# Kernel optimization log

Hardware: AMD Instinct MI355X
Metric: run time of the kernel (lower is better)

Reference implementation:

```python
import jax, jax.numpy as jnp
import numpy as np


def _dsepconv(inp, vert, horiz, offx, offy, mask):
    # inp: [B,C,H,W]; vert/horiz: [B,F,H,W]; offx/offy/mask: [B,F*F,H,W]
    B, C, H, W = inp.shape
    F = vert.shape[1]
    FF = F * F
    dt = inp.dtype
    k = jnp.arange(FF)
    ki = (k // F).astype(dt)   # vertical tap index i
    kj = (k % F).astype(dt)    # horizontal tap index j
    half = jnp.asarray((F - 1) / 2.0, dt)
    ys = jnp.arange(H, dtype=dt)
    xs = jnp.arange(W, dtype=dt)
    # per-pixel deformable sample positions, [B,FF,H,W]
    py = offy + ys[None, None, :, None] + (ki - half)[None, :, None, None]
    px = offx + xs[None, None, None, :] + (kj - half)[None, :, None, None]
    py = jnp.clip(py, 0.0, H - 1)
    px = jnp.clip(px, 0.0, W - 1)
    y0f = jnp.floor(py)
    x0f = jnp.floor(px)
    wy = py - y0f   # bilinear fractional weights
    wx = px - x0f
    y0 = y0f.astype(jnp.int32)
    x0 = x0f.astype(jnp.int32)
    y1 = jnp.minimum(y0 + 1, H - 1)
    x1 = jnp.minimum(x0 + 1, W - 1)

    inp_flat = inp.reshape(B, C, H * W)

    def gather(yi, xi):
        # flat spatial gather per batch element -> [B,C,FF,H,W]
        idx = (yi * W + xi).reshape(B, FF * H * W)
        g = jax.vmap(lambda im, ix: im[:, ix])(inp_flat, idx)
        return g.reshape(B, C, FF, H, W)

    g00 = gather(y0, x0)
    g01 = gather(y0, x1)
    g10 = gather(y1, x0)
    g11 = gather(y1, x1)
    wy_ = wy[:, None]  # [B,1,FF,H,W]
    wx_ = wx[:, None]
    samp = (g00 * (1 - wy_) * (1 - wx_)
            + g01 * (1 - wy_) * wx_
            + g10 * wy_ * (1 - wx_)
            + g11 * wy_ * wx_)  # [B,C,FF,H,W]
    # separable mask-weighted tap weights: vert[i]*horiz[j]*mask[k]
    wtap = vert[:, k // F] * horiz[:, k % F] * mask  # [B,FF,H,W]
    return jnp.einsum('bkhw,bckhw->bchw', wtap, samp)


def setup_inputs() -> dict:
    key = jax.random.key(0)
    ks = jax.random.split(key, 6)
    B, C, H, W, F = 4, 3, 384, 384, 5
    return {
        'tensorInput': jax.random.normal(ks[0], (B, C, H, W), jnp.float32),
        'tensorVertical': jax.random.uniform(ks[1], (B, F, H, W), jnp.float32),
        'tensorHorizontal': jax.random.uniform(ks[2], (B, F, H, W), jnp.float32),
        'tensorOffsetX': jax.random.normal(ks[3], (B, F * F, H, W), jnp.float32),
        'tensorOffsetY': jax.random.normal(ks[4], (B, F * F, H, W), jnp.float32),
        'tensorMask': jax.random.uniform(ks[5], (B, F * F, H, W), jnp.float32),
    }


def reference(tensorInput, tensorVertical, tensorHorizontal, tensorOffsetX, tensorOffsetY, tensorMask):
    return _dsepconv(tensorInput, tensorVertical, tensorHorizontal,
                     tensorOffsetX, tensorOffsetY, tensorMask)
```

## Files before the change

### kernel.cpp

```cpp
#include <hip/hip_runtime.h>

#define BB 4
#define CC 3
#define HH 384
#define WW 384
#define FF 5
#define KK 25
#define HW (HH*WW)

#define TX 32
#define TY 8

typedef float fx4 __attribute__((ext_vector_type(4)));

__device__ __forceinline__ fx4 nt_load4(const float* p) {
    return __builtin_nontemporal_load((const fx4*)p);
}

__global__ __launch_bounds__(256) void transpose_kernel(
    const float* __restrict__ inp, float4* __restrict__ wsin)
{
    int t = blockIdx.x * blockDim.x + threadIdx.x;
    if (t >= BB * (HW / 4)) return;
    int b = t / (HW / 4);
    int i = (t - b * (HW / 4)) * 4;
    const float* base = inp + (size_t)b * CC * HW + i;
    fx4 c0 = nt_load4(base);
    fx4 c1 = nt_load4(base + HW);
    fx4 c2 = nt_load4(base + 2 * HW);
    float4* o = wsin + (size_t)b * HW + i;
    o[0] = make_float4(c0.x, c1.x, c2.x, 0.f);
    o[1] = make_float4(c0.y, c1.y, c2.y, 0.f);
    o[2] = make_float4(c0.z, c1.z, c2.z, 0.f);
    o[3] = make_float4(c0.w, c1.w, c2.w, 0.f);
}

__global__ __launch_bounds__(256) void dsepconv_kernel(
    const float4* __restrict__ wsin,
    const float* __restrict__ vert,
    const float* __restrict__ horiz,
    const float* __restrict__ offx,
    const float* __restrict__ offy,
    const float* __restrict__ mask,
    float* __restrict__ out)
{
    int tx = threadIdx.x & (TX - 1);
    int ty = threadIdx.x / TX;
    int x = blockIdx.x * TX + tx;
    int y = blockIdx.y * TY + ty;
    int b = blockIdx.z;
    int planeoff = y * WW + x;

    float v[FF], hz[FF];
#pragma unroll
    for (int f = 0; f < FF; ++f) {
        v[f]  = __builtin_nontemporal_load(vert  + (b * FF + f) * HW + planeoff);
        hz[f] = __builtin_nontemporal_load(horiz + (b * FF + f) * HW + planeoff);
    }

    const float4* in_b = wsin + (size_t)b * HW;

    float acc0 = 0.f, acc1 = 0.f, acc2 = 0.f;
    const float fy = (float)y;
    const float fx = (float)x;

    for (int ki = 0; ki < FF; ++ki) {
        float vki = v[ki];
        float dy  = fy + (float)(ki - 2);
        const float* ox_p = offx + (size_t)(b * KK + ki * FF) * HW + planeoff;
        const float* oy_p = offy + (size_t)(b * KK + ki * FF) * HW + planeoff;
        const float* m_p  = mask + (size_t)(b * KK + ki * FF) * HW + planeoff;
#pragma unroll
        for (int kj = 0; kj < FF; ++kj) {
            float ox = __builtin_nontemporal_load(ox_p + kj * HW);
            float oy = __builtin_nontemporal_load(oy_p + kj * HW);
            float m  = __builtin_nontemporal_load(m_p  + kj * HW);
            float wt = vki * hz[kj] * m;

            float py = oy + dy;
            float px = ox + fx + (float)(kj - 2);
            py = fminf(fmaxf(py, 0.f), (float)(HH - 1));
            px = fminf(fmaxf(px, 0.f), (float)(WW - 1));
            float y0f = floorf(py);
            float x0f = floorf(px);
            float wy = py - y0f;
            float wx = px - x0f;
            int y0 = (int)y0f;
            int x0 = (int)x0f;
            int y1 = min(y0 + 1, HH - 1);
            int x1 = min(x0 + 1, WW - 1);

            float4 g00 = in_b[y0 * WW + x0];
            float4 g01 = in_b[y0 * WW + x1];
            float4 g10 = in_b[y1 * WW + x0];
            float4 g11 = in_b[y1 * WW + x1];

            float w00 = (1.f - wy) * (1.f - wx);
            float w01 = (1.f - wy) * wx;
            float w10 = wy * (1.f - wx);
            float w11 = wy * wx;

            acc0 += wt * (g00.x * w00 + g01.x * w01 + g10.x * w10 + g11.x * w11);
            acc1 += wt * (g00.y * w00 + g01.y * w01 + g10.y * w10 + g11.y * w11);
            acc2 += wt * (g00.z * w00 + g01.z * w01 + g10.z * w10 + g11.z * w11);
        }
    }

    out[(b * CC + 0) * HW + planeoff] = acc0;
    out[(b * CC + 1) * HW + planeoff] = acc1;
    out[(b * CC + 2) * HW + planeoff] = acc2;
}

extern "C" void kernel_launch(void* const* d_in, const int* in_sizes, int n_in,
                              void* d_out, int out_size, void* d_ws, size_t ws_size,
                              hipStream_t stream) {
    const float* inp   = (const float*)d_in[0];
    const float* vert  = (const float*)d_in[1];
    const float* horiz = (const float*)d_in[2];
    const float* offx  = (const float*)d_in[3];
    const float* offy  = (const float*)d_in[4];
    const float* mask  = (const float*)d_in[5];
    float* out = (float*)d_out;
    float4* wsin = (float4*)d_ws;

    {
        int total = BB * (HW / 4);
        transpose_kernel<<<(total + 255) / 256, 256, 0, stream>>>(inp, wsin);
    }
    {
        dim3 grid(WW / TX, HH / TY, BB);
        dsepconv_kernel<<<grid, 256, 0, stream>>>(
            wsin, vert, horiz, offx, offy, mask, out);
    }
}
```

Before: 253.8 us.

## Pack input as fp16 horizontal pixel pairs to halve bilinear gather loads

Replaces the fp32 channel-interleaved float4 image with an fp16 table in which each 16-byte entry holds two horizontally adjacent pixels. Two copies are stored, one for even and one for odd start columns, so each bilinear sample needs two 16-byte loads instead of four. This cuts gather instructions and cache footprint. The trade-off is fp16 rounding of the input values, which adds precision error, plus extra unpack conversions per tap.

```diff
diff --git a/kernel.cpp b/kernel.cpp
--- a/kernel.cpp
+++ b/kernel.cpp
@@ -1,4 +1,5 @@
 #include <hip/hip_runtime.h>
+#include <hip/hip_fp16.h>
 
 #define BB 4
 #define CC 3
@@ -7,36 +8,52 @@
 #define FF 5
 #define KK 25
 #define HW (HH*WW)
+#define WP 192
+#define TOT (BB*HH*WP)
 
 #define TX 32
 #define TY 8
 
-typedef float fx4 __attribute__((ext_vector_type(4)));
-
-__device__ __forceinline__ fx4 nt_load4(const float* p) {
-    return __builtin_nontemporal_load((const fx4*)p);
+__device__ __forceinline__ uint2 pack_px(float c0, float c1, float c2) {
+    __half2 h01 = __floats2half2_rn(c0, c1);
+    uint2 r;
+    r.x = *(const unsigned int*)&h01;
+    r.y = (unsigned int)__half_as_ushort(__float2half_rn(c2));
+    return r;
 }
 
-__global__ __launch_bounds__(256) void transpose_kernel(
-    const float* __restrict__ inp, float4* __restrict__ wsin)
+__global__ __launch_bounds__(256) void pack_kernel(
+    const float* __restrict__ inp, uint4* __restrict__ tab)
 {
     int t = blockIdx.x * blockDim.x + threadIdx.x;
-    if (t >= BB * (HW / 4)) return;
-    int b = t / (HW / 4);
-    int i = (t - b * (HW / 4)) * 4;
-    const float* base = inp + (size_t)b * CC * HW + i;
-    fx4 c0 = nt_load4(base);
-    fx4 c1 = nt_load4(base + HW);
-    fx4 c2 = nt_load4(base + 2 * HW);
-    float4* o = wsin + (size_t)b * HW + i;
-    o[0] = make_float4(c0.x, c1.x, c2.x, 0.f);
-    o[1] = make_float4(c0.y, c1.y, c2.y, 0.f);
-    o[2] = make_float4(c0.z, c1.z, c2.z, 0.f);
-    o[3] = make_float4(c0.w, c1.w, c2.w, 0.f);
+    if (t >= TOT) return;
+    int j = t % WP;
+    int y = (t / WP) % HH;
+    int b = t / (WP * HH);
+    int p0 = 2 * j, p1 = 2 * j + 1, p2 = min(2 * j + 2, WW - 1);
+    const float* b0 = inp + (((size_t)b * CC + 0) * HH + y) * WW;
+    const float* b1 = inp + (((size_t)b * CC + 1) * HH + y) * WW;
+    const float* b2 = inp + (((size_t)b * CC + 2) * HH + y) * WW;
+    uint2 q0 = pack_px(b0[p0], b1[p0], b2[p0]);
+    uint2 q1 = pack_px(b0[p1], b1[p1], b2[p1]);
+    uint2 q2 = pack_px(b0[p2], b1[p2], b2[p2]);
+    tab[t]       = make_uint4(q0.x, q0.y, q1.x, q1.y);
+    tab[TOT + t] = make_uint4(q1.x, q1.y, q2.x, q2.y);
+}
+
+__device__ __forceinline__ void unpack_pair(uint4 r,
+    float& lo0, float& lo1, float& lo2, float& hi0, float& hi1, float& hi2)
+{
+    float2 lo01 = __half22float2(*(const __half2*)&r.x);
+    float2 hi01 = __half22float2(*(const __half2*)&r.z);
+    lo0 = lo01.x; lo1 = lo01.y;
+    hi0 = hi01.x; hi1 = hi01.y;
+    lo2 = __half2float(*(const __half*)&r.y);
+    hi2 = __half2float(*(const __half*)&r.w);
 }
 
 __global__ __launch_bounds__(256) void dsepconv_kernel(
-    const float4* __restrict__ wsin,
+    const uint4* __restrict__ tab,
     const float* __restrict__ vert,
     const float* __restrict__ horiz,
     const float* __restrict__ offx,
@@ -58,7 +75,7 @@
         hz[f] = __builtin_nontemporal_load(horiz + (b * FF + f) * HW + planeoff);
     }
 
-    const float4* in_b = wsin + (size_t)b * HW;
+    const uint4* tb = tab + (size_t)b * (HH * WP);
 
     float acc0 = 0.f, acc1 = 0.f, acc2 = 0.f;
     const float fy = (float)y;
@@ -88,21 +105,26 @@
             int y0 = (int)y0f;
             int x0 = (int)x0f;
             int y1 = min(y0 + 1, HH - 1);
-            int x1 = min(x0 + 1, WW - 1);
 
-            float4 g00 = in_b[y0 * WW + x0];
-            float4 g01 = in_b[y0 * WW + x1];
-            float4 g10 = in_b[y1 * WW + x0];
-            float4 g11 = in_b[y1 * WW + x1];
+            int j    = x0 >> 1;
+            int selo = (x0 & 1) ? TOT : 0;
+            const uint4* tbs = tb + selo;
+            uint4 r0 = tbs[y0 * WP + j];
+            uint4 r1 = tbs[y1 * WP + j];
+
+            float a00, a01, a02, b00, b01, b02;
+            float a10, a11, a12, b10, b11, b12;
+            unpack_pair(r0, a00, a01, a02, b00, b01, b02);
+            unpack_pair(r1, a10, a11, a12, b10, b11, b12);
 
             float w00 = (1.f - wy) * (1.f - wx);
             float w01 = (1.f - wy) * wx;
             float w10 = wy * (1.f - wx);
             float w11 = wy * wx;
 
-            acc0 += wt * (g00.x * w00 + g01.x * w01 + g10.x * w10 + g11.x * w11);
-            acc1 += wt * (g00.y * w00 + g01.y * w01 + g10.y * w10 + g11.y * w11);
-            acc2 += wt * (g00.z * w00 + g01.z * w01 + g10.z * w10 + g11.z * w11);
+            acc0 += wt * (a00 * w00 + b00 * w01 + a10 * w10 + b10 * w11);
+            acc1 += wt * (a01 * w00 + b01 * w01 + a11 * w10 + b11 * w11);
+            acc2 += wt * (a02 * w00 + b02 * w01 + a12 * w10 + b12 * w11);
         }
     }
 
@@ -121,15 +143,14 @@
     const float* offy  = (const float*)d_in[4];
     const float* mask  = (const float*)d_in[5];
     float* out = (float*)d_out;
-    float4* wsin = (float4*)d_ws;
+    uint4* tab = (uint4*)d_ws;
 
     {
-        int total = BB * (HW / 4);
-        transpose_kernel<<<(total + 255) / 256, 256, 0, stream>>>(inp, wsin);
+        pack_kernel<<<(TOT + 255) / 256, 256, 0, stream>>>(inp, tab);
     }
     {
         dim3 grid(WW / TX, HH / TY, BB);
         dsepconv_kernel<<<grid, 256, 0, stream>>>(
-            wsin, vert, horiz, offx, offy, mask, out);
+            tab, vert, horiz, offx, offy, mask, out);
     }
 }
```

After: 231.9 us. 1.09x faster.
